# Kernel optimization log

Measured on AMD Instinct MI355X. Metric: run time of the kernel, lower is better.

The kernel has to match this reference:

```python
import jax, jax.numpy as jnp
import numpy as np

NUM_HEADS = 16
HEAD_DIM = 64
ROPE_BASE = 160000.0


def _rope_tables(seq_len, head_dim):
    inv_freq = 1.0 / (ROPE_BASE ** (jnp.arange(0, head_dim, 2, dtype=jnp.float32) / head_dim))
    freqs = jnp.arange(seq_len, dtype=jnp.float32)[:, None] * inv_freq[None, :]  # [S, hd/2]
    return jnp.cos(freqs)[None, None], jnp.sin(freqs)[None, None]  # [1,1,S,hd/2]


def _apply_rope(x, cos, sin):
    # x: [B, nh, S, hd]; split-half rotation as in the torch module
    x1, x2 = jnp.split(x, 2, axis=-1)
    return jnp.concatenate([x1 * cos - x2 * sin, x2 * cos + x1 * sin], axis=-1)


def setup_inputs() -> dict:
    key = jax.random.key(0)
    k1, k2, k3 = jax.random.split(key, 3)
    B, S, H = 2, 2048, 1024
    hidden_states = jax.random.normal(k1, (B, S, H), dtype=jnp.float32)
    # additive causal mask: 0 for allowed, -1e9 for future positions
    causal = jnp.tril(jnp.ones((S, S), dtype=bool))
    attention_mask = jnp.where(causal, 0.0, -1e9).astype(jnp.float32)[None, None]
    Wqkv = jax.random.normal(k2, (H, 3 * H), dtype=jnp.float32) * (H ** -0.5)
    Wo = jax.random.normal(k3, (H, H), dtype=jnp.float32) * (H ** -0.5)
    return {"hidden_states": hidden_states, "attention_mask": attention_mask, "Wqkv": Wqkv, "Wo": Wo}


def reference(hidden_states, attention_mask, Wqkv, Wo):
    B, S, H = hidden_states.shape
    nh, hd = NUM_HEADS, HEAD_DIM
    scale = hd ** -0.5

    qkv = hidden_states @ Wqkv                                   # [B,S,3H]
    qkv = qkv.reshape(B, S, 3, nh, hd).transpose(2, 0, 3, 1, 4)  # [3,B,nh,S,hd]
    q, k, v = qkv[0], qkv[1], qkv[2]

    cos, sin = _rope_tables(S, hd)
    q = _apply_rope(q, cos, sin)
    k = _apply_rope(k, cos, sin)

    scores = jnp.einsum('bhqd,bhkd->bhqk', q, k) * scale + attention_mask
    attn = jax.nn.softmax(scores, axis=-1)
    out = jnp.einsum('bhqk,bhkd->bhqd', attn, v)                 # [B,nh,S,hd]
    out = out.transpose(0, 2, 1, 3).reshape(B, S, H)
    return out @ Wo
```

## Files before the change

### kernel.cpp

```cpp
#include <hip/hip_runtime.h>
#include <hip/hip_bf16.h>

typedef __bf16 bf16x8 __attribute__((ext_vector_type(8)));
typedef float f32x4 __attribute__((ext_vector_type(4)));
typedef unsigned short u16;

__device__ __forceinline__ u16 f2bf(float f) {
    union { float f; unsigned u; } x{f};
    unsigned r = x.u + 0x7fffu + ((x.u >> 16) & 1u);
    return (u16)(r >> 16);
}
__device__ __forceinline__ float bf2f(u16 h) {
    union { unsigned u; float f; } x{(unsigned)h << 16};
    return x.f;
}
__device__ __forceinline__ unsigned pk2(float a, float b) {
    union { float f; unsigned u; } x{a}, y{b};
    return ((x.u + 0x8000u) >> 16) | ((y.u + 0x8000u) & 0xffff0000u);
}
__device__ __forceinline__ f32x4 zero4() { f32x4 z = {0.f, 0.f, 0.f, 0.f}; return z; }

__global__ void __launch_bounds__(256) cast_bf16(const float* __restrict__ x,
                                                 u16* __restrict__ y, int n4) {
    int i = (blockIdx.x * 256 + threadIdx.x) * 4;
    if (i >= n4 * 4) return;
    float4 v = *(const float4*)(x + i);
    ushort4 o;
    o.x = f2bf(v.x); o.y = f2bf(v.y); o.z = f2bf(v.z); o.w = f2bf(v.w);
    *(ushort4*)(y + i) = o;
}

__global__ void __launch_bounds__(256) transpose_cast(const float* __restrict__ W,
                                                      u16* __restrict__ Wt, int K, int N) {
    __shared__ float tile[32][33];
    int tx = threadIdx.x, ty = threadIdx.y;
    int n0 = blockIdx.x * 32, k0 = blockIdx.y * 32;
#pragma unroll
    for (int i = 0; i < 32; i += 8)
        tile[ty + i][tx] = W[(size_t)(k0 + ty + i) * N + n0 + tx];
    __syncthreads();
#pragma unroll
    for (int i = 0; i < 32; i += 8)
        Wt[(size_t)(n0 + ty + i) * K + k0 + tx] = f2bf(tile[tx][ty + i]);
}

template <typename OutT>
__global__ void __launch_bounds__(256) gemm_bt(const u16* __restrict__ A,
                                               const u16* __restrict__ Bt,
                                               OutT* __restrict__ C,
                                               int M, int N, int K) {
    __shared__ __align__(16) u16 As[128][40];
    __shared__ __align__(16) u16 Bs[128][40];
    const int t = threadIdx.x;
    const int lane = t & 63, w = t >> 6;
    const int wm = w >> 1, wn = w & 1;
    const int m16 = lane & 15, q4 = lane >> 4;
    const int bm = blockIdx.y, bn = blockIdx.x;
    const int r = t >> 1, c0 = (t & 1) * 16;

    const u16* Ag = A + (size_t)(bm * 128 + r) * K + c0;
    const u16* Bg = Bt + (size_t)(bn * 128 + r) * K + c0;

    f32x4 acc[4][4];
#pragma unroll
    for (int i = 0; i < 4; i++)
#pragma unroll
        for (int j = 0; j < 4; j++) acc[i][j] = zero4();

    for (int k0 = 0; k0 < K; k0 += 32) {
        uint4 a0 = *(const uint4*)(Ag + k0);
        uint4 a1 = *(const uint4*)(Ag + k0 + 8);
        uint4 b0 = *(const uint4*)(Bg + k0);
        uint4 b1 = *(const uint4*)(Bg + k0 + 8);
        __syncthreads();
        *(uint4*)&As[r][c0] = a0; *(uint4*)&As[r][c0 + 8] = a1;
        *(uint4*)&Bs[r][c0] = b0; *(uint4*)&Bs[r][c0 + 8] = b1;
        __syncthreads();
        bf16x8 af[4], bf[4];
#pragma unroll
        for (int i = 0; i < 4; i++)
            af[i] = *(const bf16x8*)&As[wm * 64 + i * 16 + m16][q4 * 8];
#pragma unroll
        for (int j = 0; j < 4; j++)
            bf[j] = *(const bf16x8*)&Bs[wn * 64 + j * 16 + m16][q4 * 8];
#pragma unroll
        for (int i = 0; i < 4; i++)
#pragma unroll
            for (int j = 0; j < 4; j++)
                acc[i][j] = __builtin_amdgcn_mfma_f32_16x16x32_bf16(af[i], bf[j], acc[i][j], 0, 0, 0);
    }
#pragma unroll
    for (int i = 0; i < 4; i++)
#pragma unroll
        for (int j = 0; j < 4; j++)
#pragma unroll
            for (int rr = 0; rr < 4; rr++) {
                int row = bm * 128 + wm * 64 + i * 16 + q4 * 4 + rr;
                int col = bn * 128 + wn * 64 + j * 16 + m16;
                float v = acc[i][j][rr];
                if constexpr (sizeof(OutT) == 4) {
                    C[(size_t)row * N + col] = v;
                } else {
                    C[(size_t)row * N + col] = f2bf(v);
                }
            }
}

__global__ void __launch_bounds__(256) rope_kernel(const u16* __restrict__ qkv,
                                                   u16* __restrict__ Q,
                                                   u16* __restrict__ Kd,
                                                   u16* __restrict__ V) {
    int t = blockIdx.x * 256 + threadIdx.x;
    int d = t & 31;
    int h = (t >> 5) & 15;
    int s = (t >> 9) & 2047;
    int b = t >> 20;
    size_t in_base = ((size_t)(b * 2048 + s)) * 3072 + h * 64;
    float q1 = bf2f(qkv[in_base + d]);
    float q2 = bf2f(qkv[in_base + d + 32]);
    float k1 = bf2f(qkv[in_base + 1024 + d]);
    float k2 = bf2f(qkv[in_base + 1024 + d + 32]);
    u16 v1 = qkv[in_base + 2048 + d];
    u16 v2 = qkv[in_base + 2048 + d + 32];

    const float c_log = 0.374466538f;
    float inv = expf(-(float)d * c_log);
    float th = (float)s * inv;
    float cs = cosf(th), sn = sinf(th);

    const float scale = 0.125f;
    size_t out_base = ((size_t)(b * 16 + h) * 2048 + s) * 64;
    Q[out_base + d]      = f2bf((q1 * cs - q2 * sn) * scale);
    Q[out_base + d + 32] = f2bf((q2 * cs + q1 * sn) * scale);
    Kd[out_base + d]      = f2bf(k1 * cs - k2 * sn);
    Kd[out_base + d + 32] = f2bf(k2 * cs + k1 * sn);
    V[out_base + d]      = v1;
    V[out_base + d + 32] = v2;
}

__global__ void __launch_bounds__(256) attn_kernel(const u16* __restrict__ Q,
                                                   const u16* __restrict__ Kg_,
                                                   const u16* __restrict__ Vg_,
                                                   u16* __restrict__ O) {
    __shared__ __align__(16) u16 Ks[2][64][72];
    __shared__ __align__(16) u16 Vt[2][64][72];
    __shared__ __align__(16) u16 Pt[4][16][72];
    const int t = threadIdx.x, w = t >> 6;
    const int m16 = t & 15, q4 = (t & 63) >> 4;
    const int bx = blockIdx.x, bh = blockIdx.y;
    const size_t base = (size_t)bh * 2048 * 64;
    const int b = bh >> 4, h = bh & 15;
    const int skey = t >> 2, sc = (t & 3) * 16;
    const int vkey = t & 63, vd = w * 16;

#pragma unroll 1
    for (int ph = 0; ph < 2; ph++) {
        const int qt = ph ? (31 - bx) : bx;
        const int qrow = qt * 64 + w * 16 + m16;
        const u16* Qg = Q + base + (size_t)qrow * 64;
        bf16x8 qf0 = *(const bf16x8*)(Qg + q4 * 8);
        bf16x8 qf1 = *(const bf16x8*)(Qg + 32 + q4 * 8);

        f32x4 occ[4];
#pragma unroll
        for (int dc = 0; dc < 4; dc++) occ[dc] = zero4();
        float mi = -3e38f, li = 0.f;

        const u16* Kb0 = Kg_ + base;
        const u16* Vb0 = Vg_ + base;
        uint4 ka = *(const uint4*)(Kb0 + skey * 64 + sc);
        uint4 kb = *(const uint4*)(Kb0 + skey * 64 + sc + 8);
        uint4 va = *(const uint4*)(Vb0 + vkey * 64 + vd);
        uint4 vb = *(const uint4*)(Vb0 + vkey * 64 + vd + 8);

#pragma unroll 1
        for (int jt = 0; jt <= qt; jt++) {
            const int bi = jt & 1;
            *(uint4*)&Ks[bi][skey][sc] = ka;
            *(uint4*)&Ks[bi][skey][sc + 8] = kb;
            {
                unsigned vv[8] = {va.x, va.y, va.z, va.w, vb.x, vb.y, vb.z, vb.w};
#pragma unroll
                for (int i = 0; i < 8; i++) {
                    Vt[bi][vd + 2 * i][vkey] = (u16)(vv[i] & 0xffffu);
                    Vt[bi][vd + 2 * i + 1][vkey] = (u16)(vv[i] >> 16);
                }
            }
            if (jt < qt) {
                const u16* Kn = Kb0 + (size_t)(jt + 1) * 4096;
                const u16* Vn = Vb0 + (size_t)(jt + 1) * 4096;
                ka = *(const uint4*)(Kn + skey * 64 + sc);
                kb = *(const uint4*)(Kn + skey * 64 + sc + 8);
                va = *(const uint4*)(Vn + vkey * 64 + vd);
                vb = *(const uint4*)(Vn + vkey * 64 + vd + 8);
            }
            __syncthreads();

            f32x4 st[4];
#pragma unroll
            for (int c = 0; c < 4; c++) st[c] = zero4();
#pragma unroll
            for (int c = 0; c < 4; c++) {
                bf16x8 kf0 = *(const bf16x8*)&Ks[bi][c * 16 + m16][q4 * 8];
                bf16x8 kf1 = *(const bf16x8*)&Ks[bi][c * 16 + m16][32 + q4 * 8];
                st[c] = __builtin_amdgcn_mfma_f32_16x16x32_bf16(kf0, qf0, st[c], 0, 0, 0);
                st[c] = __builtin_amdgcn_mfma_f32_16x16x32_bf16(kf1, qf1, st[c], 0, 0, 0);
            }

            float pv[4][4];
#pragma unroll
            for (int c = 0; c < 4; c++)
#pragma unroll
                for (int rr = 0; rr < 4; rr++) pv[c][rr] = st[c][rr];
            if (jt == qt) {
                const int ql = w * 16 + m16;
#pragma unroll
                for (int c = 0; c < 4; c++)
#pragma unroll
                    for (int rr = 0; rr < 4; rr++)
                        if (c * 16 + q4 * 4 + rr > ql) pv[c][rr] = -3e38f;
            }

            float mx = -3e38f;
#pragma unroll
            for (int c = 0; c < 4; c++)
#pragma unroll
                for (int rr = 0; rr < 4; rr++) mx = fmaxf(mx, pv[c][rr]);
            mx = fmaxf(mx, __shfl_xor(mx, 16));
            mx = fmaxf(mx, __shfl_xor(mx, 32));
            float mn = fmaxf(mi, mx);
            float alpha = __expf(mi - mn);
            mi = mn;
            float rs = 0.f;
#pragma unroll
            for (int c = 0; c < 4; c++) {
                float p0 = __expf(pv[c][0] - mn);
                float p1 = __expf(pv[c][1] - mn);
                float p2 = __expf(pv[c][2] - mn);
                float p3 = __expf(pv[c][3] - mn);
                rs += (p0 + p1) + (p2 + p3);
                uint2 pkd = make_uint2(pk2(p0, p1), pk2(p2, p3));
                *(uint2*)&Pt[w][m16][c * 16 + q4 * 4] = pkd;
            }
            rs += __shfl_xor(rs, 16);
            rs += __shfl_xor(rs, 32);
            li = li * alpha + rs;
#pragma unroll
            for (int dc = 0; dc < 4; dc++) {
                occ[dc][0] *= alpha; occ[dc][1] *= alpha;
                occ[dc][2] *= alpha; occ[dc][3] *= alpha;
            }

#pragma unroll
            for (int ks = 0; ks < 2; ks++) {
                bf16x8 pf = *(const bf16x8*)&Pt[w][m16][ks * 32 + q4 * 8];
#pragma unroll
                for (int dc = 0; dc < 4; dc++) {
                    bf16x8 vf = *(const bf16x8*)&Vt[bi][dc * 16 + m16][ks * 32 + q4 * 8];
                    occ[dc] = __builtin_amdgcn_mfma_f32_16x16x32_bf16(vf, pf, occ[dc], 0, 0, 0);
                }
            }
        }

        float rli = 1.0f / li;
        u16* Op = O + ((size_t)(b * 2048 + qrow)) * 1024 + h * 64 + q4 * 4;
#pragma unroll
        for (int dc = 0; dc < 4; dc++) {
            ushort4 o;
            o.x = f2bf(occ[dc][0] * rli);
            o.y = f2bf(occ[dc][1] * rli);
            o.z = f2bf(occ[dc][2] * rli);
            o.w = f2bf(occ[dc][3] * rli);
            *(ushort4*)(Op + dc * 16) = o;
        }
        __syncthreads();
    }
}

extern "C" void kernel_launch(void* const* d_in, const int* in_sizes, int n_in,
                              void* d_out, int out_size, void* d_ws, size_t ws_size,
                              hipStream_t stream) {
    const float* hs   = (const float*)d_in[0];
    const float* Wqkv = (const float*)d_in[2];
    const float* Wo   = (const float*)d_in[3];
    float* out = (float*)d_out;

    const int BS = 4096;
    const int H = 1024, N3 = 3072;
    const int SH = 32 * 2048 * 64;

    u16* Xb    = (u16*)d_ws;
    u16* Wqkvt = Xb + (size_t)BS * H;
    u16* Wot   = Wqkvt + (size_t)N3 * H;
    u16* QKVb  = Wot + (size_t)H * H;
    u16* Qb    = QKVb + (size_t)BS * N3;
    u16* Kb    = Qb + SH;
    u16* Vb    = Kb + SH;
    u16* AOb   = Vb + SH;

    cast_bf16<<<(BS * H / 4 + 255) / 256, 256, 0, stream>>>(hs, Xb, BS * H / 4);
    transpose_cast<<<dim3(N3 / 32, H / 32), dim3(32, 8), 0, stream>>>(Wqkv, Wqkvt, H, N3);
    transpose_cast<<<dim3(H / 32, H / 32), dim3(32, 8), 0, stream>>>(Wo, Wot, H, H);

    gemm_bt<u16><<<dim3(N3 / 128, BS / 128), 256, 0, stream>>>(Xb, Wqkvt, QKVb, BS, N3, H);

    rope_kernel<<<(2 * 2048 * 16 * 32) / 256, 256, 0, stream>>>(QKVb, Qb, Kb, Vb);

    attn_kernel<<<dim3(16, 32), 256, 0, stream>>>(Qb, Kb, Vb, AOb);

    gemm_bt<float><<<dim3(H / 128, BS / 128), 256, 0, stream>>>(AOb, Wot, out, BS, H, H);
}
```

Baseline: 220.3 us.

## Use async global-to-LDS loads in GEMM, pre-transpose V, and switch softmax to exp2

The GEMM now loads tiles with global_load_lds straight into an unpadded, XOR-swizzled LDS layout, dropping the register staging round-trip. A separate vtrans kernel writes V transposed into the reused QKV buffer, so the attention kernel stores V with vector writes instead of scattered 16-bit LDS stores. Softmax uses exp2 with log2(e) folded into the Q scale, and a barrier now sits at the end of each key tile. The cost is one extra kernel launch plus a V round-trip through memory, and the GEMM loses the register prefetch that hid global load latency.

```diff
diff --git a/kernel.cpp b/kernel.cpp
--- a/kernel.cpp
+++ b/kernel.cpp
@@ -18,7 +18,14 @@
     union { float f; unsigned u; } x{a}, y{b};
     return ((x.u + 0x8000u) >> 16) | ((y.u + 0x8000u) & 0xffff0000u);
 }
+__device__ __forceinline__ float ex2(float x) { return __builtin_amdgcn_exp2f(x); }
 __device__ __forceinline__ f32x4 zero4() { f32x4 z = {0.f, 0.f, 0.f, 0.f}; return z; }
+
+typedef const __attribute__((address_space(1))) unsigned int* gp1_t;
+typedef __attribute__((address_space(3))) unsigned int* lp3_t;
+__device__ __forceinline__ void async16(const u16* g, u16* l) {
+    __builtin_amdgcn_global_load_lds((gp1_t)g, (lp3_t)l, 16, 0, 0);
+}
 
 __global__ void __launch_bounds__(256) cast_bf16(const float* __restrict__ x,
                                                  u16* __restrict__ y, int n4) {
@@ -44,22 +51,44 @@
         Wt[(size_t)(n0 + ty + i) * K + k0 + tx] = f2bf(tile[tx][ty + i]);
 }
 
+__global__ void __launch_bounds__(256) vtrans(const u16* __restrict__ V,
+                                              u16* __restrict__ Vt) {
+    __shared__ u16 tile[32][33];
+    int tx = threadIdx.x, ty = threadIdx.y;
+    int s0 = blockIdx.x * 32, d0 = blockIdx.y * 32;
+    size_t bi = (size_t)blockIdx.z * 2048 * 64;
+#pragma unroll
+    for (int i = 0; i < 32; i += 8)
+        tile[ty + i][tx] = V[bi + (size_t)(s0 + ty + i) * 64 + d0 + tx];
+    __syncthreads();
+#pragma unroll
+    for (int i = 0; i < 32; i += 8)
+        Vt[bi + (size_t)(d0 + ty + i) * 2048 + s0 + tx] = tile[tx][ty + i];
+}
+
 template <typename OutT>
 __global__ void __launch_bounds__(256) gemm_bt(const u16* __restrict__ A,
                                                const u16* __restrict__ Bt,
                                                OutT* __restrict__ C,
                                                int M, int N, int K) {
-    __shared__ __align__(16) u16 As[128][40];
-    __shared__ __align__(16) u16 Bs[128][40];
+    __shared__ __align__(16) u16 As[128 * 32];
+    __shared__ __align__(16) u16 Bs[128 * 32];
     const int t = threadIdx.x;
     const int lane = t & 63, w = t >> 6;
     const int wm = w >> 1, wn = w & 1;
     const int m16 = lane & 15, q4 = lane >> 4;
     const int bm = blockIdx.y, bn = blockIdx.x;
-    const int r = t >> 1, c0 = (t & 1) * 16;
-
-    const u16* Ag = A + (size_t)(bm * 128 + r) * K + c0;
-    const u16* Bg = Bt + (size_t)(bn * 128 + r) * K + c0;
+
+    const int lrow = lane >> 2;
+    const int kchunk = (lane & 3) ^ ((lane >> 3) & 3);
+    const u16* Ag = A + (size_t)(bm * 128 + w * 32 + lrow) * K + kchunk * 8;
+    const u16* Bg = Bt + (size_t)(bn * 128 + w * 32 + lrow) * K + kchunk * 8;
+    u16* Al0 = As + (w * 32) * 32;
+    u16* Al1 = As + (w * 32 + 16) * 32;
+    u16* Bl0 = Bs + (w * 32) * 32;
+    u16* Bl1 = Bs + (w * 32 + 16) * 32;
+
+    const int kswz = (q4 ^ ((m16 >> 1) & 3)) * 8;
 
     f32x4 acc[4][4];
 #pragma unroll
@@ -68,21 +97,19 @@
         for (int j = 0; j < 4; j++) acc[i][j] = zero4();
 
     for (int k0 = 0; k0 < K; k0 += 32) {
-        uint4 a0 = *(const uint4*)(Ag + k0);
-        uint4 a1 = *(const uint4*)(Ag + k0 + 8);
-        uint4 b0 = *(const uint4*)(Bg + k0);
-        uint4 b1 = *(const uint4*)(Bg + k0 + 8);
         __syncthreads();
-        *(uint4*)&As[r][c0] = a0; *(uint4*)&As[r][c0 + 8] = a1;
-        *(uint4*)&Bs[r][c0] = b0; *(uint4*)&Bs[r][c0 + 8] = b1;
+        async16(Ag + k0, Al0);
+        async16(Ag + 16 * K + k0, Al1);
+        async16(Bg + k0, Bl0);
+        async16(Bg + 16 * K + k0, Bl1);
         __syncthreads();
         bf16x8 af[4], bf[4];
 #pragma unroll
         for (int i = 0; i < 4; i++)
-            af[i] = *(const bf16x8*)&As[wm * 64 + i * 16 + m16][q4 * 8];
+            af[i] = *(const bf16x8*)&As[(wm * 64 + i * 16 + m16) * 32 + kswz];
 #pragma unroll
         for (int j = 0; j < 4; j++)
-            bf[j] = *(const bf16x8*)&Bs[wn * 64 + j * 16 + m16][q4 * 8];
+            bf[j] = *(const bf16x8*)&Bs[(wn * 64 + j * 16 + m16) * 32 + kswz];
 #pragma unroll
         for (int i = 0; i < 4; i++)
 #pragma unroll
@@ -128,7 +155,7 @@
     float th = (float)s * inv;
     float cs = cosf(th), sn = sinf(th);
 
-    const float scale = 0.125f;
+    const float scale = 0.125f * 1.44269504f;
     size_t out_base = ((size_t)(b * 16 + h) * 2048 + s) * 64;
     Q[out_base + d]      = f2bf((q1 * cs - q2 * sn) * scale);
     Q[out_base + d + 32] = f2bf((q2 * cs + q1 * sn) * scale);
@@ -140,7 +167,7 @@
 
 __global__ void __launch_bounds__(256) attn_kernel(const u16* __restrict__ Q,
                                                    const u16* __restrict__ Kg_,
-                                                   const u16* __restrict__ Vg_,
+                                                   const u16* __restrict__ Vtg_,
                                                    u16* __restrict__ O) {
     __shared__ __align__(16) u16 Ks[2][64][72];
     __shared__ __align__(16) u16 Vt[2][64][72];
@@ -151,7 +178,6 @@
     const size_t base = (size_t)bh * 2048 * 64;
     const int b = bh >> 4, h = bh & 15;
     const int skey = t >> 2, sc = (t & 3) * 16;
-    const int vkey = t & 63, vd = w * 16;
 
 #pragma unroll 1
     for (int ph = 0; ph < 2; ph++) {
@@ -164,35 +190,29 @@
         f32x4 occ[4];
 #pragma unroll
         for (int dc = 0; dc < 4; dc++) occ[dc] = zero4();
-        float mi = -3e38f, li = 0.f;
-
-        const u16* Kb0 = Kg_ + base;
-        const u16* Vb0 = Vg_ + base;
-        uint4 ka = *(const uint4*)(Kb0 + skey * 64 + sc);
-        uint4 kb = *(const uint4*)(Kb0 + skey * 64 + sc + 8);
-        uint4 va = *(const uint4*)(Vb0 + vkey * 64 + vd);
-        uint4 vb = *(const uint4*)(Vb0 + vkey * 64 + vd + 8);
+        float mi = -1e30f, li = 0.f;
+
+        const u16* Kb0 = Kg_ + base + skey * 64 + sc;
+        const u16* Vt0 = Vtg_ + base + (size_t)skey * 2048 + sc;
+        uint4 ka = *(const uint4*)(Kb0);
+        uint4 kb = *(const uint4*)(Kb0 + 8);
+        uint4 va = *(const uint4*)(Vt0);
+        uint4 vb = *(const uint4*)(Vt0 + 8);
 
 #pragma unroll 1
         for (int jt = 0; jt <= qt; jt++) {
             const int bi = jt & 1;
             *(uint4*)&Ks[bi][skey][sc] = ka;
             *(uint4*)&Ks[bi][skey][sc + 8] = kb;
-            {
-                unsigned vv[8] = {va.x, va.y, va.z, va.w, vb.x, vb.y, vb.z, vb.w};
-#pragma unroll
-                for (int i = 0; i < 8; i++) {
-                    Vt[bi][vd + 2 * i][vkey] = (u16)(vv[i] & 0xffffu);
-                    Vt[bi][vd + 2 * i + 1][vkey] = (u16)(vv[i] >> 16);
-                }
-            }
+            *(uint4*)&Vt[bi][skey][sc] = va;
+            *(uint4*)&Vt[bi][skey][sc + 8] = vb;
             if (jt < qt) {
                 const u16* Kn = Kb0 + (size_t)(jt + 1) * 4096;
-                const u16* Vn = Vb0 + (size_t)(jt + 1) * 4096;
-                ka = *(const uint4*)(Kn + skey * 64 + sc);
-                kb = *(const uint4*)(Kn + skey * 64 + sc + 8);
-                va = *(const uint4*)(Vn + vkey * 64 + vd);
-                vb = *(const uint4*)(Vn + vkey * 64 + vd + 8);
+                const u16* Vn = Vt0 + (size_t)(jt + 1) * 64;
+                ka = *(const uint4*)(Kn);
+                kb = *(const uint4*)(Kn + 8);
+                va = *(const uint4*)(Vn);
+                vb = *(const uint4*)(Vn + 8);
             }
             __syncthreads();
 
@@ -218,10 +238,10 @@
                 for (int c = 0; c < 4; c++)
 #pragma unroll
                     for (int rr = 0; rr < 4; rr++)
-                        if (c * 16 + q4 * 4 + rr > ql) pv[c][rr] = -3e38f;
-            }
-
-            float mx = -3e38f;
+                        if (c * 16 + q4 * 4 + rr > ql) pv[c][rr] = -1e30f;
+            }
+
+            float mx = -1e30f;
 #pragma unroll
             for (int c = 0; c < 4; c++)
 #pragma unroll
@@ -229,15 +249,15 @@
             mx = fmaxf(mx, __shfl_xor(mx, 16));
             mx = fmaxf(mx, __shfl_xor(mx, 32));
             float mn = fmaxf(mi, mx);
-            float alpha = __expf(mi - mn);
+            float alpha = ex2(mi - mn);
             mi = mn;
             float rs = 0.f;
 #pragma unroll
             for (int c = 0; c < 4; c++) {
-                float p0 = __expf(pv[c][0] - mn);
-                float p1 = __expf(pv[c][1] - mn);
-                float p2 = __expf(pv[c][2] - mn);
-                float p3 = __expf(pv[c][3] - mn);
+                float p0 = ex2(pv[c][0] - mn);
+                float p1 = ex2(pv[c][1] - mn);
+                float p2 = ex2(pv[c][2] - mn);
+                float p3 = ex2(pv[c][3] - mn);
                 rs += (p0 + p1) + (p2 + p3);
                 uint2 pkd = make_uint2(pk2(p0, p1), pk2(p2, p3));
                 *(uint2*)&Pt[w][m16][c * 16 + q4 * 4] = pkd;
@@ -260,6 +280,7 @@
                     occ[dc] = __builtin_amdgcn_mfma_f32_16x16x32_bf16(vf, pf, occ[dc], 0, 0, 0);
                 }
             }
+            __syncthreads();
         }
 
         float rli = 1.0f / li;
@@ -273,7 +294,6 @@
             o.w = f2bf(occ[dc][3] * rli);
             *(ushort4*)(Op + dc * 16) = o;
         }
-        __syncthreads();
     }
 }
 
@@ -297,6 +317,7 @@
     u16* Kb    = Qb + SH;
     u16* Vb    = Kb + SH;
     u16* AOb   = Vb + SH;
+    u16* Vtg   = QKVb;
 
     cast_bf16<<<(BS * H / 4 + 255) / 256, 256, 0, stream>>>(hs, Xb, BS * H / 4);
     transpose_cast<<<dim3(N3 / 32, H / 32), dim3(32, 8), 0, stream>>>(Wqkv, Wqkvt, H, N3);
@@ -306,7 +327,9 @@
 
     rope_kernel<<<(2 * 2048 * 16 * 32) / 256, 256, 0, stream>>>(QKVb, Qb, Kb, Vb);
 
-    attn_kernel<<<dim3(16, 32), 256, 0, stream>>>(Qb, Kb, Vb, AOb);
+    vtrans<<<dim3(64, 2, 32), dim3(32, 8), 0, stream>>>(Vb, Vtg);
+
+    attn_kernel<<<dim3(16, 32), 256, 0, stream>>>(Qb, Kb, Vtg, AOb);
 
     gemm_bt<float><<<dim3(H / 128, BS / 128), 256, 0, stream>>>(AOb, Wot, out, BS, H, H);
 }
```

Result: no change. 218.8 us (-0.6%).
